# Performance work log

Measured on AMD Instinct MI355X. Metric: run time of the kernel, lower is better.

## Reference

```python
import jax, jax.numpy as jnp
import numpy as np

H = W = 32
CROP = int(H * 0.8)  # 25, matches int(H*crop_ratio) in torch
MEAN = jnp.array([0.5071, 0.4867, 0.4408], jnp.float32).reshape(1, 3, 1, 1)
STD = jnp.array([0.2675, 0.2565, 0.2761], jnp.float32).reshape(1, 3, 1, 1)


def _bilinear(img, iy, ix):
    # img [C,H,W]; iy/ix [H,W] float pixel coords (reflected+clamped already)
    y0 = jnp.floor(iy); x0 = jnp.floor(ix)
    wy = iy - y0; wx = ix - x0
    y0i = jnp.clip(y0.astype(jnp.int32), 0, H - 1); y1i = jnp.clip(y0i + 1, 0, H - 1)
    x0i = jnp.clip(x0.astype(jnp.int32), 0, W - 1); x1i = jnp.clip(x0i + 1, 0, W - 1)
    v00 = img[:, y0i, x0i]; v01 = img[:, y0i, x1i]
    v10 = img[:, y1i, x0i]; v11 = img[:, y1i, x1i]
    return v00 * (1 - wy) * (1 - wx) + v01 * (1 - wy) * wx + v10 * wy * (1 - wx) + v11 * wy * wx


def _reflect(c, size):
    # PyTorch grid_sample reflection padding, align_corners=False (reflect about -0.5 / size-0.5)
    lo = -0.5
    span = float(size)
    t = jnp.abs(c - lo)
    extra = jnp.mod(t, span)
    flips = jnp.floor(t / span)
    out = jnp.where(jnp.mod(flips, 2.0) == 0.0, lo + extra, lo + span - extra)
    return jnp.clip(out, 0.0, size - 1.0)


def _crop_resize_one(img, top, left):
    # bilinear resize of img[:, top:top+CROP, left:left+CROP] -> HxW, align_corners=False
    d = (jnp.arange(W, dtype=jnp.float32) + 0.5) * (CROP / W) - 0.5
    d = jnp.maximum(d, 0.0)
    i0 = jnp.floor(d).astype(jnp.int32)
    lam = d - i0
    i1 = jnp.minimum(i0 + 1, CROP - 1)
    r0 = top + i0; r1 = top + i1; c0 = left + i0; c1 = left + i1
    v00 = img[:, r0[:, None], c0[None, :]]
    v01 = img[:, r0[:, None], c1[None, :]]
    v10 = img[:, r1[:, None], c0[None, :]]
    v11 = img[:, r1[:, None], c1[None, :]]
    ly = lam[:, None]; lx = lam[None, :]
    return v00 * (1 - ly) * (1 - lx) + v01 * (1 - ly) * lx + v10 * ly * (1 - lx) + v11 * ly * lx


def _grid_sample_one(img, theta):
    # affine_grid + grid_sample (bilinear, reflection, align_corners=False)
    xs = (2.0 * (jnp.arange(W, dtype=jnp.float32) + 0.5) / W) - 1.0
    ys = (2.0 * (jnp.arange(H, dtype=jnp.float32) + 0.5) / H) - 1.0
    yn, xn = jnp.meshgrid(ys, xs, indexing='ij')
    gx = theta[0, 0] * xn + theta[0, 1] * yn + theta[0, 2]
    gy = theta[1, 0] * xn + theta[1, 1] * yn + theta[1, 2]
    ix = _reflect(((gx + 1.0) * W - 1.0) * 0.5, W)
    iy = _reflect(((gy + 1.0) * H - 1.0) * 0.5, H)
    return _bilinear(img, iy, ix)


def _augment(x, shared_affine, apply_crop):
    B = x.shape[0]
    ks = jax.random.split(jax.random.key(42), 10)
    x = x * STD + MEAN  # de-normalize
    if apply_crop:
        max_off = H - CROP
        top = jax.random.randint(ks[0], (B,), 0, max_off + 1)
        left = jax.random.randint(ks[1], (B,), 0, max_off + 1)
        x = jax.vmap(_crop_resize_one)(x, top, left)
    flip_mask = jax.random.uniform(ks[2], (B,)) < 0.5
    x = jnp.where(flip_mask[:, None, None, None], x[..., ::-1], x)
    # shared affine is provided -> always applied (torch shared_affine branch)
    x = jax.vmap(_grid_sample_one)(x, shared_affine)
    brightness = 1.0 + (jax.random.uniform(ks[3], (B, 1, 1, 1)) - 0.5) * 0.8
    x = x * brightness
    gray = x.mean(axis=1, keepdims=True)
    contrast = 1.0 + (jax.random.uniform(ks[4], (B, 1, 1, 1)) - 0.5) * 0.8
    x = gray + (x - gray) * contrast
    gray = x.mean(axis=1, keepdims=True)
    saturation = 1.0 + (jax.random.uniform(ks[5], (B, 1, 1, 1)) - 0.5) * 0.8
    x = gray + (x - gray) * saturation
    hue_mask = jax.random.uniform(ks[6], (B,)) < 0.5
    x = jnp.where(hue_mask[:, None, None, None], x[:, ::-1], x)  # BGR swap
    gray_mask = jax.random.uniform(ks[7], (B,)) < 0.2
    x = jnp.where(gray_mask[:, None, None, None], x.mean(axis=1, keepdims=True), x)
    blur_mask = jax.random.uniform(ks[8], (B,)) < 0.5
    xp = jnp.pad(x, ((0, 0), (0, 0), (1, 1), (1, 1)), mode='edge')  # replicate pad
    bl = sum(xp[:, :, i:i + H, j:j + W] for i in range(3) for j in range(3)) / 9.0  # 3x3 box blur
    x = jnp.where(blur_mask[:, None, None, None], bl, x)
    solar_mask = jax.random.uniform(ks[9], (B,)) < 0.1
    x = jnp.where(solar_mask[:, None, None, None] & (x > 0.5), 1.0 - x, x)
    x = jnp.clip(x, 0.0, 1.0)
    x = (x - MEAN) / STD  # re-normalize
    return x, flip_mask


def setup_inputs() -> dict:
    key = jax.random.key(0)
    k1, k2 = jax.random.split(key)
    B = 8192
    x = jax.random.normal(k1, (B, 3, H, W), jnp.float32)
    eye = jnp.broadcast_to(jnp.array([[1.0, 0.0, 0.0], [0.0, 1.0, 0.0]], jnp.float32), (B, 2, 3))
    shared_affine = eye + 0.1 * jax.random.normal(k2, (B, 2, 3), jnp.float32)
    return {"x": x, "shared_affine": shared_affine, "apply_crop": 1}


def reference(x, shared_affine, apply_crop):
    out, flip_mask = _augment(x, shared_affine, int(apply_crop))
    # torch returns (x, {'flip': flip_mask, 'affine': affine_theta})
    return out, flip_mask, shared_affine
```

## Files before the change

kernel.cpp:

```cpp
#include <hip/hip_runtime.h>

#define HW 32
#define NPIX 1024
#define IMG 3072

typedef float vf4 __attribute__((ext_vector_type(4)));

__device__ __forceinline__ unsigned rotl32(unsigned x, int d) {
    return (x << d) | (x >> (32 - d));
}

struct UPair { unsigned a, b; };

__device__ __forceinline__ UPair threefry2x32(unsigned k0, unsigned k1,
                                              unsigned x0, unsigned x1) {
    unsigned k2 = k0 ^ k1 ^ 0x1BD11BDAu;
    x0 += k0; x1 += k1;
#define RND(r) { x0 += x1; x1 = rotl32(x1, (r)); x1 ^= x0; }
    RND(13) RND(15) RND(26) RND(6)
    x0 += k1; x1 += k2 + 1u;
    RND(17) RND(29) RND(16) RND(24)
    x0 += k2; x1 += k0 + 2u;
    RND(13) RND(15) RND(26) RND(6)
    x0 += k0; x1 += k1 + 3u;
    RND(17) RND(29) RND(16) RND(24)
    x0 += k1; x1 += k2 + 4u;
    RND(13) RND(15) RND(26) RND(6)
    x0 += k2; x1 += k0 + 5u;
#undef RND
    return {x0, x1};
}

__device__ __forceinline__ float bits_to_u01(unsigned bits) {
    return __uint_as_float((bits >> 9) | 0x3f800000u) - 1.0f;
}

__device__ __forceinline__ float reflect32(float c) {
    float t = fabsf(c + 0.5f);
    float flips = floorf(t * 0.03125f);
    float extra = fmaf(flips, -32.0f, t);
    float o = (((int)flips) & 1) ? (31.5f - extra) : (extra - 0.5f);
    return fminf(fmaxf(o, 0.0f), 31.0f);
}

__device__ __forceinline__ float rfl_f(float v) {
    return __uint_as_float(__builtin_amdgcn_readfirstlane(__float_as_uint(v)));
}
__device__ __forceinline__ int rfl_i(int v) {
    return __builtin_amdgcn_readfirstlane(v);
}

__global__ __launch_bounds__(256) void aug_kernel(
    const float* __restrict__ xin, const float* __restrict__ aff,
    const int* __restrict__ apply_crop, float* __restrict__ out, int B) {
    __shared__ vf4 buf[NPIX];
    __shared__ float s_theta[6];
    __shared__ int s_top, s_left, s_flip, s_hue, s_gray, s_blur, s_solar;
    __shared__ float s_bright, s_contr, s_sat;

    const int b = blockIdx.x;
    const int t = threadIdx.x;
    const int x = t & 31;
    const int yr = t >> 5;
    const bool do_crop = (apply_crop[0] != 0);

    const float* src = xin + (size_t)b * IMG;
    float g0[4], g1[4], g2[4];
#pragma unroll
    for (int i = 0; i < 4; ++i) {
        int p = t + 256 * i;
        g0[i] = src[p];
        g1[i] = src[NPIX + p];
        g2[i] = src[2 * NPIX + p];
    }

    const size_t OUT_IMG = (size_t)B * IMG;
    if (t < 6) {
        float v = aff[b * 6 + t];
        s_theta[t] = v;
        out[OUT_IMG + (size_t)B + (size_t)b * 6 + t] = v;
    }

    if (t < 10) {
        int k = t;
        UPair K = threefry2x32(0u, 42u, 0u, (unsigned)k);
        if (k < 2) {
            UPair k2 = threefry2x32(K.a, K.b, 0u, 1u);
            UPair r = threefry2x32(k2.a, k2.b, 0u, (unsigned)b);
            int val = (int)((r.a ^ r.b) & 7u);
            if (k == 0) s_top = val; else s_left = val;
        } else {
            UPair r = threefry2x32(K.a, K.b, 0u, (unsigned)b);
            float u = bits_to_u01(r.a ^ r.b);
            if      (k == 2) s_flip  = (u < 0.5f);
            else if (k == 3) s_bright = 1.0f + (u - 0.5f) * 0.8f;
            else if (k == 4) s_contr  = 1.0f + (u - 0.5f) * 0.8f;
            else if (k == 5) s_sat    = 1.0f + (u - 0.5f) * 0.8f;
            else if (k == 6) s_hue   = (u < 0.5f);
            else if (k == 7) s_gray  = (u < 0.2f);
            else if (k == 8) s_blur  = (u < 0.5f);
            else             s_solar = (u < 0.1f);
        }
    }

#pragma unroll
    for (int i = 0; i < 4; ++i) {
        vf4 v;
        v.x = fmaf(g0[i], 0.2675f, 0.5071f);
        v.y = fmaf(g1[i], 0.2565f, 0.4867f);
        v.z = fmaf(g2[i], 0.2761f, 0.4408f);
        v.w = 0.0f;
        buf[t + 256 * i] = v;
    }
    __syncthreads();

    if (t == 0) out[OUT_IMG + b] = s_flip ? 1.0f : 0.0f;
    const int top  = rfl_i(s_top),  left = rfl_i(s_left);
    const int flip = rfl_i(s_flip), hue  = rfl_i(s_hue);
    const int gray = rfl_i(s_gray), blur = rfl_i(s_blur), solar = rfl_i(s_solar);
    const float br   = rfl_f(s_bright);
    const float ctsa = rfl_f(s_contr) * rfl_f(s_sat);
    const float th0 = rfl_f(s_theta[0]), th1 = rfl_f(s_theta[1]), th2 = rfl_f(s_theta[2]);
    const float th3 = rfl_f(s_theta[3]), th4 = rfl_f(s_theta[4]), th5 = rfl_f(s_theta[5]);

    float cx[4], cy[4], cz[4];

    if (do_crop) {
        float dxv = fmaxf(fmaf((float)x, 0.78125f, -0.109375f), 0.0f);
        int q0 = (int)dxv; float lx = dxv - (float)q0; int q1 = min(q0 + 1, 24);
        int c0 = left + q0, c1 = left + q1;
        float omx = 1.0f - lx;
#pragma unroll
        for (int i = 0; i < 4; ++i) {
            int yi = yr + 8 * i;
            float dy = fmaxf(fmaf((float)yi, 0.78125f, -0.109375f), 0.0f);
            int i0 = (int)dy; float ly = dy - (float)i0; int i1 = min(i0 + 1, 24);
            int r0 = (top + i0) << 5, r1 = (top + i1) << 5;
            float omy = 1.0f - ly;
            float w00 = omy * omx, w01 = omy * lx;
            float w10 = ly * omx, w11 = ly * lx;
            vf4 t00 = buf[r0 + c0], t01 = buf[r0 + c1];
            vf4 t10 = buf[r1 + c0], t11 = buf[r1 + c1];
            cx[i] = fmaf(t00.x, w00, fmaf(t01.x, w01, fmaf(t10.x, w10, t11.x * w11)));
            cy[i] = fmaf(t00.y, w00, fmaf(t01.y, w01, fmaf(t10.y, w10, t11.y * w11)));
            cz[i] = fmaf(t00.z, w00, fmaf(t01.z, w01, fmaf(t10.z, w10, t11.z * w11)));
        }
        __syncthreads();
#pragma unroll
        for (int i = 0; i < 4; ++i) {
            vf4 v; v.x = cx[i]; v.y = cy[i]; v.z = cz[i]; v.w = 0.0f;
            buf[t + 256 * i] = v;
        }
        __syncthreads();
    }

    {
        float xn = (float)x * 0.0625f - 0.96875f;
#pragma unroll
        for (int i = 0; i < 4; ++i) {
            int yi = yr + 8 * i;
            float yn = (float)yi * 0.0625f - 0.96875f;
            float gx = fmaf(th0, xn, fmaf(th1, yn, th2));
            float gy = fmaf(th3, xn, fmaf(th4, yn, th5));
            float ix = reflect32(fmaf(gx, 16.0f, 15.5f));
            float iy = reflect32(fmaf(gy, 16.0f, 15.5f));
            float fy = floorf(iy), fx = floorf(ix);
            float wy = iy - fy, wx = ix - fx;
            int y0 = (int)fy; int y1 = min(y0 + 1, 31);
            int x0 = (int)fx; int x1 = min(x0 + 1, 31);
            if (flip) { x0 = 31 - x0; x1 = 31 - x1; }
            int r0 = y0 << 5, r1 = y1 << 5;
            float omy = 1.0f - wy, omx = 1.0f - wx;
            float w00 = omy * omx, w01 = omy * wx;
            float w10 = wy * omx, w11 = wy * wx;
            vf4 t00 = buf[r0 + x0], t01 = buf[r0 + x1];
            vf4 t10 = buf[r1 + x0], t11 = buf[r1 + x1];
            float ch0 = fmaf(t00.x, w00, fmaf(t01.x, w01, fmaf(t10.x, w10, t11.x * w11)));
            float ch1 = fmaf(t00.y, w00, fmaf(t01.y, w01, fmaf(t10.y, w10, t11.y * w11)));
            float ch2 = fmaf(t00.z, w00, fmaf(t01.z, w01, fmaf(t10.z, w10, t11.z * w11)));
            ch0 *= br; ch1 *= br; ch2 *= br;
            float g = (ch0 + ch1 + ch2) * (1.0f / 3.0f);
            ch0 = fmaf(ch0 - g, ctsa, g);
            ch1 = fmaf(ch1 - g, ctsa, g);
            ch2 = fmaf(ch2 - g, ctsa, g);
            if (hue) { float tmp = ch0; ch0 = ch2; ch2 = tmp; }
            if (gray) { ch0 = ch1 = ch2 = g; }
            cx[i] = ch0; cy[i] = ch1; cz[i] = ch2;
        }
    }

    if (blur) {
        __syncthreads();
        const int tl = t - 1, tr = t + 1;
        float hx[4], hy[4], hz[4];
#pragma unroll
        for (int i = 0; i < 4; ++i) {
            float v, lf, rt;
            v = cx[i]; lf = __shfl(v, tl); rt = __shfl(v, tr);
            if (x == 0) lf = v;  if (x == 31) rt = v;
            hx[i] = lf + v + rt;
            v = cy[i]; lf = __shfl(v, tl); rt = __shfl(v, tr);
            if (x == 0) lf = v;  if (x == 31) rt = v;
            hy[i] = lf + v + rt;
            v = cz[i]; lf = __shfl(v, tl); rt = __shfl(v, tr);
            if (x == 0) lf = v;  if (x == 31) rt = v;
            hz[i] = lf + v + rt;
        }
#pragma unroll
        for (int i = 0; i < 4; ++i) {
            vf4 v; v.x = hx[i]; v.y = hy[i]; v.z = hz[i]; v.w = 0.0f;
            buf[t + 256 * i] = v;
        }
        __syncthreads();
#pragma unroll
        for (int i = 0; i < 4; ++i) {
            int yi = yr + 8 * i;
            vf4 up = buf[(max(yi - 1, 0) << 5) + x];
            vf4 dn = buf[(min(yi + 1, 31) << 5) + x];
            cx[i] = (up.x + hx[i] + dn.x) * (1.0f / 9.0f);
            cy[i] = (up.y + hy[i] + dn.y) * (1.0f / 9.0f);
            cz[i] = (up.z + hz[i] + dn.z) * (1.0f / 9.0f);
        }
    }

    {
        const float INV0 = 1.0f / 0.2675f, INV1 = 1.0f / 0.2565f, INV2 = 1.0f / 0.2761f;
        float* o = out + (size_t)b * IMG;
#pragma unroll
        for (int i = 0; i < 4; ++i) {
            int p = t + 256 * i;
            float r0v = cx[i], r1v = cy[i], r2v = cz[i];
            if (solar) {
                if (r0v > 0.5f) r0v = 1.0f - r0v;
                if (r1v > 0.5f) r1v = 1.0f - r1v;
                if (r2v > 0.5f) r2v = 1.0f - r2v;
            }
            r0v = fminf(fmaxf(r0v, 0.0f), 1.0f);
            r1v = fminf(fmaxf(r1v, 0.0f), 1.0f);
            r2v = fminf(fmaxf(r2v, 0.0f), 1.0f);
            o[p]             = (r0v - 0.5071f) * INV0;
            o[NPIX + p]      = (r1v - 0.4867f) * INV1;
            o[2 * NPIX + p]  = (r2v - 0.4408f) * INV2;
        }
    }
}

extern "C" void kernel_launch(void* const* d_in, const int* in_sizes, int n_in,
                              void* d_out, int out_size, void* d_ws, size_t ws_size,
                              hipStream_t stream) {
    const float* x = (const float*)d_in[0];
    const float* aff = (const float*)d_in[1];
    const int* ac = (const int*)d_in[2];
    float* out = (float*)d_out;
    int B = in_sizes[0] / IMG;
    aug_kernel<<<dim3(B), dim3(256), 0, stream>>>(x, aff, ac, out, B);
}
```

Measured before the change: 182.3 us.

## Process eight images per block with prefetch and double-buffered shared memory

Each block now loops over several images instead of one. The next image's global loads and RNG parameters are issued before the current image is processed, so load latency overlaps with compute. Two shared buffers alternate roles, which removes one barrier in the crop path, and per-thread crop and grid coordinates are hoisted out of the loop. In exchange the grid shrinks to B/8 blocks, which lowers available parallelism and occupancy-based latency hiding, and the conditional barrier logic makes the buffer-reuse ordering harder to check.

Measured after the change: 208.8 us. 14.5% more time.

```diff
diff --git a/kernel.cpp b/kernel.cpp
--- a/kernel.cpp
+++ b/kernel.cpp
@@ -3,6 +3,7 @@
 #define HW 32
 #define NPIX 1024
 #define IMG 3072
+#define IPB 8
 
 typedef float vf4 __attribute__((ext_vector_type(4)));
 
@@ -53,115 +54,144 @@
 __global__ __launch_bounds__(256) void aug_kernel(
     const float* __restrict__ xin, const float* __restrict__ aff,
     const int* __restrict__ apply_crop, float* __restrict__ out, int B) {
-    __shared__ vf4 buf[NPIX];
-    __shared__ float s_theta[6];
-    __shared__ int s_top, s_left, s_flip, s_hue, s_gray, s_blur, s_solar;
-    __shared__ float s_bright, s_contr, s_sat;
-
-    const int b = blockIdx.x;
+    __shared__ vf4 bufA[NPIX];
+    __shared__ vf4 bufB[NPIX];
+    __shared__ float s_pf[2][9];
+    __shared__ int   s_pi[2][7];
+
     const int t = threadIdx.x;
     const int x = t & 31;
     const int yr = t >> 5;
     const bool do_crop = (apply_crop[0] != 0);
-
-    const float* src = xin + (size_t)b * IMG;
+    const size_t OUT_IMG = (size_t)B * IMG;
+    const int img0 = blockIdx.x * IPB;
+
+    float dxv = fmaxf(fmaf((float)x, 0.78125f, -0.109375f), 0.0f);
+    const int q0 = (int)dxv; const float lx = dxv - (float)q0;
+    const int q1 = min(q0 + 1, 24);
+    const float omx_c = 1.0f - lx;
+    const float xn = (float)x * 0.0625f - 0.96875f;
+    int i0a[4], i1a[4]; float lya[4], yna[4];
+#pragma unroll
+    for (int i = 0; i < 4; ++i) {
+        int yi = yr + 8 * i;
+        float dy = fmaxf(fmaf((float)yi, 0.78125f, -0.109375f), 0.0f);
+        i0a[i] = (int)dy; lya[i] = dy - (float)i0a[i];
+        i1a[i] = min(i0a[i] + 1, 24);
+        yna[i] = (float)yi * 0.0625f - 0.96875f;
+    }
+
+    auto compute_params = [&](int bb, int slot) {
+        if (t < 6) s_pf[slot][t] = aff[(size_t)bb * 6 + t];
+        if (t < 10) {
+            int kk = t;
+            UPair K = threefry2x32(0u, 42u, 0u, (unsigned)kk);
+            if (kk < 2) {
+                UPair k2 = threefry2x32(K.a, K.b, 0u, 1u);
+                UPair r = threefry2x32(k2.a, k2.b, 0u, (unsigned)bb);
+                s_pi[slot][kk] = (int)((r.a ^ r.b) & 7u);
+            } else {
+                UPair r = threefry2x32(K.a, K.b, 0u, (unsigned)bb);
+                float u = bits_to_u01(r.a ^ r.b);
+                if      (kk == 2) s_pi[slot][2] = (u < 0.5f);
+                else if (kk == 3) s_pf[slot][6] = 1.0f + (u - 0.5f) * 0.8f;
+                else if (kk == 4) s_pf[slot][7] = 1.0f + (u - 0.5f) * 0.8f;
+                else if (kk == 5) s_pf[slot][8] = 1.0f + (u - 0.5f) * 0.8f;
+                else if (kk == 6) s_pi[slot][3] = (u < 0.5f);
+                else if (kk == 7) s_pi[slot][4] = (u < 0.2f);
+                else if (kk == 8) s_pi[slot][5] = (u < 0.5f);
+                else              s_pi[slot][6] = (u < 0.1f);
+            }
+        }
+    };
+
     float g0[4], g1[4], g2[4];
-#pragma unroll
-    for (int i = 0; i < 4; ++i) {
-        int p = t + 256 * i;
-        g0[i] = src[p];
-        g1[i] = src[NPIX + p];
-        g2[i] = src[2 * NPIX + p];
+    {
+        const float* src = xin + (size_t)img0 * IMG;
+#pragma unroll
+        for (int i = 0; i < 4; ++i) {
+            int p = t + 256 * i;
+            g0[i] = src[p]; g1[i] = src[NPIX + p]; g2[i] = src[2 * NPIX + p];
+        }
     }
-
-    const size_t OUT_IMG = (size_t)B * IMG;
-    if (t < 6) {
-        float v = aff[b * 6 + t];
-        s_theta[t] = v;
-        out[OUT_IMG + (size_t)B + (size_t)b * 6 + t] = v;
-    }
-
-    if (t < 10) {
-        int k = t;
-        UPair K = threefry2x32(0u, 42u, 0u, (unsigned)k);
-        if (k < 2) {
-            UPair k2 = threefry2x32(K.a, K.b, 0u, 1u);
-            UPair r = threefry2x32(k2.a, k2.b, 0u, (unsigned)b);
-            int val = (int)((r.a ^ r.b) & 7u);
-            if (k == 0) s_top = val; else s_left = val;
+    compute_params(img0, 0);
+    __syncthreads();
+
+    for (int k = 0; k < IPB; ++k) {
+        const int b = img0 + k;
+        if (b >= B) break;
+        const int par = k & 1;
+        vf4* S = par ? bufB : bufA;
+        vf4* C = par ? bufA : bufB;
+
+#pragma unroll
+        for (int i = 0; i < 4; ++i) {
+            vf4 v;
+            v.x = fmaf(g0[i], 0.2675f, 0.5071f);
+            v.y = fmaf(g1[i], 0.2565f, 0.4867f);
+            v.z = fmaf(g2[i], 0.2761f, 0.4408f);
+            v.w = 0.0f;
+            S[t + 256 * i] = v;
+        }
+
+        if (k + 1 < IPB && b + 1 < B) {
+            const float* src = xin + (size_t)(b + 1) * IMG;
+#pragma unroll
+            for (int i = 0; i < 4; ++i) {
+                int p = t + 256 * i;
+                g0[i] = src[p]; g1[i] = src[NPIX + p]; g2[i] = src[2 * NPIX + p];
+            }
+            compute_params(b + 1, par ^ 1);
+        }
+
+        if (t == 0) out[OUT_IMG + b] = s_pi[par][2] ? 1.0f : 0.0f;
+        if (t < 6)  out[OUT_IMG + (size_t)B + (size_t)b * 6 + t] = s_pf[par][t];
+
+        __syncthreads();
+
+        const int top  = rfl_i(s_pi[par][0]), left = rfl_i(s_pi[par][1]);
+        const int flip = rfl_i(s_pi[par][2]), hue  = rfl_i(s_pi[par][3]);
+        const int gray = rfl_i(s_pi[par][4]), blur = rfl_i(s_pi[par][5]);
+        const int solar = rfl_i(s_pi[par][6]);
+        const float br   = rfl_f(s_pf[par][6]);
+        const float ctsa = rfl_f(s_pf[par][7]) * rfl_f(s_pf[par][8]);
+        const float th0 = rfl_f(s_pf[par][0]), th1 = rfl_f(s_pf[par][1]);
+        const float th2 = rfl_f(s_pf[par][2]), th3 = rfl_f(s_pf[par][3]);
+        const float th4 = rfl_f(s_pf[par][4]), th5 = rfl_f(s_pf[par][5]);
+
+        vf4* cur;
+        vf4* freeb;
+        float cx[4], cy[4], cz[4];
+
+        if (do_crop) {
+            const int c0 = left + q0, c1 = left + q1;
+#pragma unroll
+            for (int i = 0; i < 4; ++i) {
+                int r0 = (top + i0a[i]) << 5, r1 = (top + i1a[i]) << 5;
+                float ly = lya[i], omy = 1.0f - ly;
+                float w00 = omy * omx_c, w01 = omy * lx;
+                float w10 = ly * omx_c, w11 = ly * lx;
+                vf4 t00 = S[r0 + c0], t01 = S[r0 + c1];
+                vf4 t10 = S[r1 + c0], t11 = S[r1 + c1];
+                cx[i] = fmaf(t00.x, w00, fmaf(t01.x, w01, fmaf(t10.x, w10, t11.x * w11)));
+                cy[i] = fmaf(t00.y, w00, fmaf(t01.y, w01, fmaf(t10.y, w10, t11.y * w11)));
+                cz[i] = fmaf(t00.z, w00, fmaf(t01.z, w01, fmaf(t10.z, w10, t11.z * w11)));
+            }
+#pragma unroll
+            for (int i = 0; i < 4; ++i) {
+                vf4 v; v.x = cx[i]; v.y = cy[i]; v.z = cz[i]; v.w = 0.0f;
+                C[t + 256 * i] = v;
+            }
+            __syncthreads();
+            cur = C; freeb = S;
         } else {
-            UPair r = threefry2x32(K.a, K.b, 0u, (unsigned)b);
-            float u = bits_to_u01(r.a ^ r.b);
-            if      (k == 2) s_flip  = (u < 0.5f);
-            else if (k == 3) s_bright = 1.0f + (u - 0.5f) * 0.8f;
-            else if (k == 4) s_contr  = 1.0f + (u - 0.5f) * 0.8f;
-            else if (k == 5) s_sat    = 1.0f + (u - 0.5f) * 0.8f;
-            else if (k == 6) s_hue   = (u < 0.5f);
-            else if (k == 7) s_gray  = (u < 0.2f);
-            else if (k == 8) s_blur  = (u < 0.5f);
-            else             s_solar = (u < 0.1f);
-        }
-    }
-
-#pragma unroll
-    for (int i = 0; i < 4; ++i) {
-        vf4 v;
-        v.x = fmaf(g0[i], 0.2675f, 0.5071f);
-        v.y = fmaf(g1[i], 0.2565f, 0.4867f);
-        v.z = fmaf(g2[i], 0.2761f, 0.4408f);
-        v.w = 0.0f;
-        buf[t + 256 * i] = v;
-    }
-    __syncthreads();
-
-    if (t == 0) out[OUT_IMG + b] = s_flip ? 1.0f : 0.0f;
-    const int top  = rfl_i(s_top),  left = rfl_i(s_left);
-    const int flip = rfl_i(s_flip), hue  = rfl_i(s_hue);
-    const int gray = rfl_i(s_gray), blur = rfl_i(s_blur), solar = rfl_i(s_solar);
-    const float br   = rfl_f(s_bright);
-    const float ctsa = rfl_f(s_contr) * rfl_f(s_sat);
-    const float th0 = rfl_f(s_theta[0]), th1 = rfl_f(s_theta[1]), th2 = rfl_f(s_theta[2]);
-    const float th3 = rfl_f(s_theta[3]), th4 = rfl_f(s_theta[4]), th5 = rfl_f(s_theta[5]);
-
-    float cx[4], cy[4], cz[4];
-
-    if (do_crop) {
-        float dxv = fmaxf(fmaf((float)x, 0.78125f, -0.109375f), 0.0f);
-        int q0 = (int)dxv; float lx = dxv - (float)q0; int q1 = min(q0 + 1, 24);
-        int c0 = left + q0, c1 = left + q1;
-        float omx = 1.0f - lx;
+            cur = S; freeb = C;
+        }
+
 #pragma unroll
         for (int i = 0; i < 4; ++i) {
-            int yi = yr + 8 * i;
-            float dy = fmaxf(fmaf((float)yi, 0.78125f, -0.109375f), 0.0f);
-            int i0 = (int)dy; float ly = dy - (float)i0; int i1 = min(i0 + 1, 24);
-            int r0 = (top + i0) << 5, r1 = (top + i1) << 5;
-            float omy = 1.0f - ly;
-            float w00 = omy * omx, w01 = omy * lx;
-            float w10 = ly * omx, w11 = ly * lx;
-            vf4 t00 = buf[r0 + c0], t01 = buf[r0 + c1];
-            vf4 t10 = buf[r1 + c0], t11 = buf[r1 + c1];
-            cx[i] = fmaf(t00.x, w00, fmaf(t01.x, w01, fmaf(t10.x, w10, t11.x * w11)));
-            cy[i] = fmaf(t00.y, w00, fmaf(t01.y, w01, fmaf(t10.y, w10, t11.y * w11)));
-            cz[i] = fmaf(t00.z, w00, fmaf(t01.z, w01, fmaf(t10.z, w10, t11.z * w11)));
-        }
-        __syncthreads();
-#pragma unroll
-        for (int i = 0; i < 4; ++i) {
-            vf4 v; v.x = cx[i]; v.y = cy[i]; v.z = cz[i]; v.w = 0.0f;
-            buf[t + 256 * i] = v;
-        }
-        __syncthreads();
-    }
-
-    {
-        float xn = (float)x * 0.0625f - 0.96875f;
-#pragma unroll
-        for (int i = 0; i < 4; ++i) {
-            int yi = yr + 8 * i;
-            float yn = (float)yi * 0.0625f - 0.96875f;
-            float gx = fmaf(th0, xn, fmaf(th1, yn, th2));
-            float gy = fmaf(th3, xn, fmaf(th4, yn, th5));
+            float gx = fmaf(th0, xn, fmaf(th1, yna[i], th2));
+            float gy = fmaf(th3, xn, fmaf(th4, yna[i], th5));
             float ix = reflect32(fmaf(gx, 16.0f, 15.5f));
             float iy = reflect32(fmaf(gy, 16.0f, 15.5f));
             float fy = floorf(iy), fx = floorf(ix);
@@ -173,8 +203,8 @@
             float omy = 1.0f - wy, omx = 1.0f - wx;
             float w00 = omy * omx, w01 = omy * wx;
             float w10 = wy * omx, w11 = wy * wx;
-            vf4 t00 = buf[r0 + x0], t01 = buf[r0 + x1];
-            vf4 t10 = buf[r1 + x0], t11 = buf[r1 + x1];
+            vf4 t00 = cur[r0 + x0], t01 = cur[r0 + x1];
+            vf4 t10 = cur[r1 + x0], t11 = cur[r1 + x1];
             float ch0 = fmaf(t00.x, w00, fmaf(t01.x, w01, fmaf(t10.x, w10, t11.x * w11)));
             float ch1 = fmaf(t00.y, w00, fmaf(t01.y, w01, fmaf(t10.y, w10, t11.y * w11)));
             float ch2 = fmaf(t00.z, w00, fmaf(t01.z, w01, fmaf(t10.z, w10, t11.z * w11)));
@@ -187,61 +217,62 @@
             if (gray) { ch0 = ch1 = ch2 = g; }
             cx[i] = ch0; cy[i] = ch1; cz[i] = ch2;
         }
-    }
-
-    if (blur) {
-        __syncthreads();
-        const int tl = t - 1, tr = t + 1;
-        float hx[4], hy[4], hz[4];
-#pragma unroll
-        for (int i = 0; i < 4; ++i) {
-            float v, lf, rt;
-            v = cx[i]; lf = __shfl(v, tl); rt = __shfl(v, tr);
-            if (x == 0) lf = v;  if (x == 31) rt = v;
-            hx[i] = lf + v + rt;
-            v = cy[i]; lf = __shfl(v, tl); rt = __shfl(v, tr);
-            if (x == 0) lf = v;  if (x == 31) rt = v;
-            hy[i] = lf + v + rt;
-            v = cz[i]; lf = __shfl(v, tl); rt = __shfl(v, tr);
-            if (x == 0) lf = v;  if (x == 31) rt = v;
-            hz[i] = lf + v + rt;
-        }
-#pragma unroll
-        for (int i = 0; i < 4; ++i) {
-            vf4 v; v.x = hx[i]; v.y = hy[i]; v.z = hz[i]; v.w = 0.0f;
-            buf[t + 256 * i] = v;
-        }
-        __syncthreads();
-#pragma unroll
-        for (int i = 0; i < 4; ++i) {
-            int yi = yr + 8 * i;
-            vf4 up = buf[(max(yi - 1, 0) << 5) + x];
-            vf4 dn = buf[(min(yi + 1, 31) << 5) + x];
-            cx[i] = (up.x + hx[i] + dn.x) * (1.0f / 9.0f);
-            cy[i] = (up.y + hy[i] + dn.y) * (1.0f / 9.0f);
-            cz[i] = (up.z + hz[i] + dn.z) * (1.0f / 9.0f);
-        }
-    }
-
-    {
-        const float INV0 = 1.0f / 0.2675f, INV1 = 1.0f / 0.2565f, INV2 = 1.0f / 0.2761f;
-        float* o = out + (size_t)b * IMG;
-#pragma unroll
-        for (int i = 0; i < 4; ++i) {
-            int p = t + 256 * i;
-            float r0v = cx[i], r1v = cy[i], r2v = cz[i];
-            if (solar) {
-                if (r0v > 0.5f) r0v = 1.0f - r0v;
-                if (r1v > 0.5f) r1v = 1.0f - r1v;
-                if (r2v > 0.5f) r2v = 1.0f - r2v;
-            }
-            r0v = fminf(fmaxf(r0v, 0.0f), 1.0f);
-            r1v = fminf(fmaxf(r1v, 0.0f), 1.0f);
-            r2v = fminf(fmaxf(r2v, 0.0f), 1.0f);
-            o[p]             = (r0v - 0.5071f) * INV0;
-            o[NPIX + p]      = (r1v - 0.4867f) * INV1;
-            o[2 * NPIX + p]  = (r2v - 0.4408f) * INV2;
-        }
+
+        if (blur) {
+            const int tl = t - 1, tr = t + 1;
+            float hx[4], hy[4], hz[4];
+#pragma unroll
+            for (int i = 0; i < 4; ++i) {
+                float v, lf, rt;
+                v = cx[i]; lf = __shfl(v, tl); rt = __shfl(v, tr);
+                if (x == 0) lf = v;  if (x == 31) rt = v;
+                hx[i] = lf + v + rt;
+                v = cy[i]; lf = __shfl(v, tl); rt = __shfl(v, tr);
+                if (x == 0) lf = v;  if (x == 31) rt = v;
+                hy[i] = lf + v + rt;
+                v = cz[i]; lf = __shfl(v, tl); rt = __shfl(v, tr);
+                if (x == 0) lf = v;  if (x == 31) rt = v;
+                hz[i] = lf + v + rt;
+            }
+#pragma unroll
+            for (int i = 0; i < 4; ++i) {
+                vf4 v; v.x = hx[i]; v.y = hy[i]; v.z = hz[i]; v.w = 0.0f;
+                freeb[t + 256 * i] = v;
+            }
+            __syncthreads();
+#pragma unroll
+            for (int i = 0; i < 4; ++i) {
+                int yi = yr + 8 * i;
+                vf4 up = freeb[(max(yi - 1, 0) << 5) + x];
+                vf4 dn = freeb[(min(yi + 1, 31) << 5) + x];
+                cx[i] = (up.x + hx[i] + dn.x) * (1.0f / 9.0f);
+                cy[i] = (up.y + hy[i] + dn.y) * (1.0f / 9.0f);
+                cz[i] = (up.z + hz[i] + dn.z) * (1.0f / 9.0f);
+            }
+        }
+
+        {
+            const float INV0 = 1.0f / 0.2675f, INV1 = 1.0f / 0.2565f, INV2 = 1.0f / 0.2761f;
+            float* o = out + (size_t)b * IMG;
+#pragma unroll
+            for (int i = 0; i < 4; ++i) {
+                int p = t + 256 * i;
+                float r0v = cx[i], r1v = cy[i], r2v = cz[i];
+                if (solar) {
+                    if (r0v > 0.5f) r0v = 1.0f - r0v;
+                    if (r1v > 0.5f) r1v = 1.0f - r1v;
+                    if (r2v > 0.5f) r2v = 1.0f - r2v;
+                }
+                r0v = fminf(fmaxf(r0v, 0.0f), 1.0f);
+                r1v = fminf(fmaxf(r1v, 0.0f), 1.0f);
+                r2v = fminf(fmaxf(r2v, 0.0f), 1.0f);
+                o[p]            = (r0v - 0.5071f) * INV0;
+                o[NPIX + p]     = (r1v - 0.4867f) * INV1;
+                o[2 * NPIX + p] = (r2v - 0.4408f) * INV2;
+            }
+        }
+
+        if (!(do_crop && blur)) __syncthreads();
     }
 }
 
@@ -253,5 +284,6 @@
     const int* ac = (const int*)d_in[2];
     float* out = (float*)d_out;
     int B = in_sizes[0] / IMG;
-    aug_kernel<<<dim3(B), dim3(256), 0, stream>>>(x, aff, ac, out, B);
-}
+    int grid = (B + IPB - 1) / IPB;
+    aug_kernel<<<dim3(grid), dim3(256), 0, stream>>>(x, aff, ac, out, B);
+}
```

## Process each image with a single wavefront, replacing barriers with shuffles

Applied to the files above, without the earlier changes.

Shrinks the block from 256 to 64 threads, so one wavefront handles a whole image at 16 pixels per thread. All __syncthreads calls go away, because LDS ordering within one wave is enough. The per-image random parameters are broadcast with lane shuffles instead of shared-memory scalars, and theta is read directly from global memory. The horizontal blur pass now reads neighbours from LDS instead of shuffling. In exchange, register pressure per thread rises, and fewer waves per CU fit within the LDS budget, which may reduce latency hiding for this memory-bound kernel.

After: 191.7 us. 1.05x slower.

```diff
diff --git a/kernel.cpp b/kernel.cpp
--- a/kernel.cpp
+++ b/kernel.cpp
@@ -43,87 +43,72 @@
     return fminf(fmaxf(o, 0.0f), 31.0f);
 }
 
-__device__ __forceinline__ float rfl_f(float v) {
-    return __uint_as_float(__builtin_amdgcn_readfirstlane(__float_as_uint(v)));
-}
-__device__ __forceinline__ int rfl_i(int v) {
-    return __builtin_amdgcn_readfirstlane(v);
-}
-
-__global__ __launch_bounds__(256) void aug_kernel(
+__global__ __launch_bounds__(64) void aug_kernel(
     const float* __restrict__ xin, const float* __restrict__ aff,
     const int* __restrict__ apply_crop, float* __restrict__ out, int B) {
     __shared__ vf4 buf[NPIX];
-    __shared__ float s_theta[6];
-    __shared__ int s_top, s_left, s_flip, s_hue, s_gray, s_blur, s_solar;
-    __shared__ float s_bright, s_contr, s_sat;
 
     const int b = blockIdx.x;
-    const int t = threadIdx.x;
-    const int x = t & 31;
-    const int yr = t >> 5;
+    const int l = threadIdx.x;
+    const int x = l & 31;
+    const int yb = l >> 5;
     const bool do_crop = (apply_crop[0] != 0);
+    const size_t OUT_IMG = (size_t)B * IMG;
+
+    const float th0 = aff[b * 6 + 0], th1 = aff[b * 6 + 1], th2 = aff[b * 6 + 2];
+    const float th3 = aff[b * 6 + 3], th4 = aff[b * 6 + 4], th5 = aff[b * 6 + 5];
 
     const float* src = xin + (size_t)b * IMG;
-    float g0[4], g1[4], g2[4];
-#pragma unroll
-    for (int i = 0; i < 4; ++i) {
-        int p = t + 256 * i;
+    float g0[16], g1[16], g2[16];
+#pragma unroll
+    for (int i = 0; i < 16; ++i) {
+        int p = l + 64 * i;
         g0[i] = src[p];
         g1[i] = src[NPIX + p];
         g2[i] = src[2 * NPIX + p];
     }
 
-    const size_t OUT_IMG = (size_t)B * IMG;
-    if (t < 6) {
-        float v = aff[b * 6 + t];
-        s_theta[t] = v;
-        out[OUT_IMG + (size_t)B + (size_t)b * 6 + t] = v;
-    }
-
-    if (t < 10) {
-        int k = t;
-        UPair K = threefry2x32(0u, 42u, 0u, (unsigned)k);
-        if (k < 2) {
+    float fval = 0.0f; int ival = 0;
+    if (l < 10) {
+        UPair K = threefry2x32(0u, 42u, 0u, (unsigned)l);
+        if (l < 2) {
             UPair k2 = threefry2x32(K.a, K.b, 0u, 1u);
             UPair r = threefry2x32(k2.a, k2.b, 0u, (unsigned)b);
-            int val = (int)((r.a ^ r.b) & 7u);
-            if (k == 0) s_top = val; else s_left = val;
+            ival = (int)((r.a ^ r.b) & 7u);
         } else {
             UPair r = threefry2x32(K.a, K.b, 0u, (unsigned)b);
             float u = bits_to_u01(r.a ^ r.b);
-            if      (k == 2) s_flip  = (u < 0.5f);
-            else if (k == 3) s_bright = 1.0f + (u - 0.5f) * 0.8f;
-            else if (k == 4) s_contr  = 1.0f + (u - 0.5f) * 0.8f;
-            else if (k == 5) s_sat    = 1.0f + (u - 0.5f) * 0.8f;
-            else if (k == 6) s_hue   = (u < 0.5f);
-            else if (k == 7) s_gray  = (u < 0.2f);
-            else if (k == 8) s_blur  = (u < 0.5f);
-            else             s_solar = (u < 0.1f);
-        }
-    }
-
-#pragma unroll
-    for (int i = 0; i < 4; ++i) {
+            if      (l == 2) ival = (u < 0.5f);
+            else if (l == 3) fval = 1.0f + (u - 0.5f) * 0.8f;
+            else if (l == 4) fval = 1.0f + (u - 0.5f) * 0.8f;
+            else if (l == 5) fval = 1.0f + (u - 0.5f) * 0.8f;
+            else if (l == 6) ival = (u < 0.5f);
+            else if (l == 7) ival = (u < 0.2f);
+            else if (l == 8) ival = (u < 0.5f);
+            else             ival = (u < 0.1f);
+        }
+    }
+    const int top  = __shfl(ival, 0), left = __shfl(ival, 1);
+    const int flip = __shfl(ival, 2), hue  = __shfl(ival, 6);
+    const int gray = __shfl(ival, 7), blur = __shfl(ival, 8);
+    const int solar = __shfl(ival, 9);
+    const float br   = __shfl(fval, 3);
+    const float ctsa = __shfl(fval, 4) * __shfl(fval, 5);
+
+    if (l == 0) out[OUT_IMG + b] = flip ? 1.0f : 0.0f;
+    if (l < 6)  out[OUT_IMG + (size_t)B + (size_t)b * 6 + l] = aff[b * 6 + l];
+
+#pragma unroll
+    for (int i = 0; i < 16; ++i) {
         vf4 v;
         v.x = fmaf(g0[i], 0.2675f, 0.5071f);
         v.y = fmaf(g1[i], 0.2565f, 0.4867f);
         v.z = fmaf(g2[i], 0.2761f, 0.4408f);
         v.w = 0.0f;
-        buf[t + 256 * i] = v;
-    }
-    __syncthreads();
-
-    if (t == 0) out[OUT_IMG + b] = s_flip ? 1.0f : 0.0f;
-    const int top  = rfl_i(s_top),  left = rfl_i(s_left);
-    const int flip = rfl_i(s_flip), hue  = rfl_i(s_hue);
-    const int gray = rfl_i(s_gray), blur = rfl_i(s_blur), solar = rfl_i(s_solar);
-    const float br   = rfl_f(s_bright);
-    const float ctsa = rfl_f(s_contr) * rfl_f(s_sat);
-    const float th0 = rfl_f(s_theta[0]), th1 = rfl_f(s_theta[1]), th2 = rfl_f(s_theta[2]);
-    const float th3 = rfl_f(s_theta[3]), th4 = rfl_f(s_theta[4]), th5 = rfl_f(s_theta[5]);
-
-    float cx[4], cy[4], cz[4];
+        buf[l + 64 * i] = v;
+    }
+
+    float cx[16], cy[16], cz[16];
 
     if (do_crop) {
         float dxv = fmaxf(fmaf((float)x, 0.78125f, -0.109375f), 0.0f);
@@ -131,9 +116,9 @@
         int c0 = left + q0, c1 = left + q1;
         float omx = 1.0f - lx;
 #pragma unroll
-        for (int i = 0; i < 4; ++i) {
-            int yi = yr + 8 * i;
-            float dy = fmaxf(fmaf((float)yi, 0.78125f, -0.109375f), 0.0f);
+        for (int i = 0; i < 16; ++i) {
+            int y = yb + 2 * i;
+            float dy = fmaxf(fmaf((float)y, 0.78125f, -0.109375f), 0.0f);
             int i0 = (int)dy; float ly = dy - (float)i0; int i1 = min(i0 + 1, 24);
             int r0 = (top + i0) << 5, r1 = (top + i1) << 5;
             float omy = 1.0f - ly;
@@ -145,21 +130,19 @@
             cy[i] = fmaf(t00.y, w00, fmaf(t01.y, w01, fmaf(t10.y, w10, t11.y * w11)));
             cz[i] = fmaf(t00.z, w00, fmaf(t01.z, w01, fmaf(t10.z, w10, t11.z * w11)));
         }
-        __syncthreads();
-#pragma unroll
-        for (int i = 0; i < 4; ++i) {
+#pragma unroll
+        for (int i = 0; i < 16; ++i) {
             vf4 v; v.x = cx[i]; v.y = cy[i]; v.z = cz[i]; v.w = 0.0f;
-            buf[t + 256 * i] = v;
-        }
-        __syncthreads();
+            buf[l + 64 * i] = v;
+        }
     }
 
     {
-        float xn = (float)x * 0.0625f - 0.96875f;
-#pragma unroll
-        for (int i = 0; i < 4; ++i) {
-            int yi = yr + 8 * i;
-            float yn = (float)yi * 0.0625f - 0.96875f;
+        const float xn = (float)x * 0.0625f - 0.96875f;
+#pragma unroll
+        for (int i = 0; i < 16; ++i) {
+            int y = yb + 2 * i;
+            float yn = (float)y * 0.0625f - 0.96875f;
             float gx = fmaf(th0, xn, fmaf(th1, yn, th2));
             float gy = fmaf(th3, xn, fmaf(th4, yn, th5));
             float ix = reflect32(fmaf(gx, 16.0f, 15.5f));
@@ -190,36 +173,34 @@
     }
 
     if (blur) {
-        __syncthreads();
-        const int tl = t - 1, tr = t + 1;
-        float hx[4], hy[4], hz[4];
-#pragma unroll
-        for (int i = 0; i < 4; ++i) {
-            float v, lf, rt;
-            v = cx[i]; lf = __shfl(v, tl); rt = __shfl(v, tr);
-            if (x == 0) lf = v;  if (x == 31) rt = v;
-            hx[i] = lf + v + rt;
-            v = cy[i]; lf = __shfl(v, tl); rt = __shfl(v, tr);
-            if (x == 0) lf = v;  if (x == 31) rt = v;
-            hy[i] = lf + v + rt;
-            v = cz[i]; lf = __shfl(v, tl); rt = __shfl(v, tr);
-            if (x == 0) lf = v;  if (x == 31) rt = v;
-            hz[i] = lf + v + rt;
-        }
-#pragma unroll
-        for (int i = 0; i < 4; ++i) {
-            vf4 v; v.x = hx[i]; v.y = hy[i]; v.z = hz[i]; v.w = 0.0f;
-            buf[t + 256 * i] = v;
-        }
-        __syncthreads();
-#pragma unroll
-        for (int i = 0; i < 4; ++i) {
-            int yi = yr + 8 * i;
-            vf4 up = buf[(max(yi - 1, 0) << 5) + x];
-            vf4 dn = buf[(min(yi + 1, 31) << 5) + x];
-            cx[i] = (up.x + hx[i] + dn.x) * (1.0f / 9.0f);
-            cy[i] = (up.y + hy[i] + dn.y) * (1.0f / 9.0f);
-            cz[i] = (up.z + hz[i] + dn.z) * (1.0f / 9.0f);
+#pragma unroll
+        for (int i = 0; i < 16; ++i) {
+            vf4 v; v.x = cx[i]; v.y = cy[i]; v.z = cz[i]; v.w = 0.0f;
+            buf[l + 64 * i] = v;
+        }
+        const int xm = max(x - 1, 0), xp = min(x + 1, 31);
+#pragma unroll
+        for (int i = 0; i < 16; ++i) {
+            int yc = (yb + 2 * i) << 5;
+            vf4 lf = buf[yc + xm];
+            vf4 rt = buf[yc + xp];
+            cx[i] = lf.x + cx[i] + rt.x;
+            cy[i] = lf.y + cy[i] + rt.y;
+            cz[i] = lf.z + cz[i] + rt.z;
+        }
+#pragma unroll
+        for (int i = 0; i < 16; ++i) {
+            vf4 v; v.x = cx[i]; v.y = cy[i]; v.z = cz[i]; v.w = 0.0f;
+            buf[l + 64 * i] = v;
+        }
+#pragma unroll
+        for (int i = 0; i < 16; ++i) {
+            int y = yb + 2 * i;
+            vf4 up = buf[(max(y - 1, 0) << 5) + x];
+            vf4 dn = buf[(min(y + 1, 31) << 5) + x];
+            cx[i] = (up.x + cx[i] + dn.x) * (1.0f / 9.0f);
+            cy[i] = (up.y + cy[i] + dn.y) * (1.0f / 9.0f);
+            cz[i] = (up.z + cz[i] + dn.z) * (1.0f / 9.0f);
         }
     }
 
@@ -227,8 +208,8 @@
         const float INV0 = 1.0f / 0.2675f, INV1 = 1.0f / 0.2565f, INV2 = 1.0f / 0.2761f;
         float* o = out + (size_t)b * IMG;
 #pragma unroll
-        for (int i = 0; i < 4; ++i) {
-            int p = t + 256 * i;
+        for (int i = 0; i < 16; ++i) {
+            int p = l + 64 * i;
             float r0v = cx[i], r1v = cy[i], r2v = cz[i];
             if (solar) {
                 if (r0v > 0.5f) r0v = 1.0f - r0v;
@@ -238,9 +219,9 @@
             r0v = fminf(fmaxf(r0v, 0.0f), 1.0f);
             r1v = fminf(fmaxf(r1v, 0.0f), 1.0f);
             r2v = fminf(fmaxf(r2v, 0.0f), 1.0f);
-            o[p]             = (r0v - 0.5071f) * INV0;
-            o[NPIX + p]      = (r1v - 0.4867f) * INV1;
-            o[2 * NPIX + p]  = (r2v - 0.4408f) * INV2;
+            o[p]            = (r0v - 0.5071f) * INV0;
+            o[NPIX + p]     = (r1v - 0.4867f) * INV1;
+            o[2 * NPIX + p] = (r2v - 0.4408f) * INV2;
         }
     }
 }
@@ -253,5 +234,5 @@
     const int* ac = (const int*)d_in[2];
     float* out = (float*)d_out;
     int B = in_sizes[0] / IMG;
-    aug_kernel<<<dim3(B), dim3(256), 0, stream>>>(x, aff, ac, out, B);
-}
+    aug_kernel<<<dim3(B), dim3(64), 0, stream>>>(x, aff, ac, out, B);
+}
```
